# Kernel optimization log

Measured on AMD Instinct MI355X. Metric: run time of the kernel, lower is better.

Reference implementation:

```python
import jax, jax.numpy as jnp
import numpy as np

B, N = 4, 65536
NUM_GROUP, GROUP_SIZE = 512, 64
EMB = 60


def setup_inputs() -> dict:
    key = jax.random.key(0)
    ks = jax.random.split(key, 8)
    inp = {
        'xyz': jax.random.uniform(ks[0], (B, N, 3), jnp.float32),
        'color': jax.random.uniform(ks[1], (B, N, 3), jnp.float32),
        'W1': jax.random.normal(ks[2], (6, 64), jnp.float32) * 0.2,
        'b1': jnp.zeros((64,), jnp.float32),
        'W2': jax.random.normal(ks[3], (64, 128), jnp.float32) * 0.1,
        'b2': jnp.zeros((128,), jnp.float32),
        'W3': jax.random.normal(ks[4], (128, 256), jnp.float32) * 0.08,
        'b3': jnp.zeros((256,), jnp.float32),
        'W4': jax.random.normal(ks[5], (256, 512), jnp.float32) * 0.06,
        'b4': jnp.zeros((512,), jnp.float32),
        'Wp': jax.random.normal(ks[6], (512, EMB), jnp.float32) * 0.04,
        'bp': jnp.zeros((EMB,), jnp.float32),
    }
    return inp


def fps(xyz, n):
    """Farthest point sampling. xyz: (B,N,3) -> centers (B,n,3)."""
    b, npts, _ = xyz.shape
    start = jnp.zeros((b,), jnp.int32)
    d0 = jnp.full((b, npts), 1e10, xyz.dtype)

    def step(carry, _):
        dists, last = carry
        p = jnp.take_along_axis(xyz, last[:, None, None], axis=1)  # (B,1,3)
        d = jnp.sum((xyz - p) ** 2, axis=-1)                       # (B,N)
        dists = jnp.minimum(dists, d)
        nxt = jnp.argmax(dists, axis=-1).astype(jnp.int32)
        return (dists, nxt), nxt

    (_, _), rest = jax.lax.scan(step, (d0, start), None, length=n - 1)
    idx = jnp.concatenate([start[:, None], rest.T], axis=1)        # (B,n)
    return jax.vmap(lambda pts, i: pts[i])(xyz, idx)


def knn_idx(k, xyz, new_xyz):
    """Indices of k nearest points in xyz for each query in new_xyz.
    xyz: (B,N,3), new_xyz: (B,S,3) -> (B,S,k) int32. Matches
    square_distance + topk(largest=False)."""
    sq = (jnp.sum(new_xyz ** 2, -1)[..., None]
          + jnp.sum(xyz ** 2, -1)[:, None, :]
          - 2.0 * jnp.einsum('bsc,bnc->bsn', new_xyz, xyz))        # (B,S,N)
    _, idx = jax.lax.top_k(-sq, k)
    return idx


def reference(xyz, color, W1, b1, W2, b2, W3, b3, W4, b4, Wp, bp):
    # --- Group: FPS centers + KNN neighborhood gather + centering ---
    center = fps(xyz, NUM_GROUP)                                   # (B,G,3)
    idx = knn_idx(GROUP_SIZE, xyz, center)                         # (B,G,M)
    gather = jax.vmap(lambda pts, i: pts[i])                       # pts[(B,)N,3], i (G,M)
    neighborhood = gather(xyz, idx) - center[:, :, None, :]        # (B,G,M,3) centered
    neighborhood_color = gather(color, idx)                        # (B,G,M,3)
    feats = jnp.concatenate([neighborhood, neighborhood_color], -1)  # (B,G,M,6)

    # --- PointNet: per-point MLP -> max over group -> projection ---
    x = jax.nn.relu(feats @ W1 + b1)
    x = jax.nn.relu(x @ W2 + b2)
    x = jax.nn.relu(x @ W3 + b3)
    x = jax.nn.relu(x @ W4 + b4)                                   # (B,G,M,512)
    x = jnp.max(x, axis=2)                                         # (B,G,512)
    emb = x @ Wp + bp                                              # (B,G,60)
    return emb, center
```

## Files before the change

kernel.cpp:

```cpp
#include <hip/hip_runtime.h>
#include <stdint.h>

#define DI __device__ __forceinline__

typedef _Float16 f16x8 __attribute__((ext_vector_type(8)));
typedef float f32x4 __attribute__((ext_vector_type(4)));

constexpr int kB = 4;
constexpr int kN = 65536;
constexpr int kG = 512;
constexpr int kM = 64;
constexpr int kE = 60;
constexpr int GRD = 20;
constexpr int NCELL = GRD * GRD * GRD;
constexpr float CW = 1.0f / 20.0f;

constexpr int FPS_SUB = 8;
constexpr int FPS_PT_T = kN / FPS_SUB / 1024;

constexpr size_t OFF_WIN    = 0;
constexpr size_t OFF_CNT    = OFF_WIN + (size_t)kB * kG * 8;
constexpr size_t OFF_CCNT   = OFF_CNT + (size_t)kB * kG * 4;
constexpr size_t ZERO_BYTES = OFF_CCNT + (size_t)kB * NCELL * 4;
constexpr size_t OFF_CSTART = ZERO_BYTES;
constexpr size_t OFF_CUR    = OFF_CSTART + (size_t)kB * (NCELL + 1) * 4;
constexpr size_t OFF_SW1    = ((OFF_CUR + (size_t)kB * NCELL * 4) + 255) & ~(size_t)255;
constexpr size_t OFF_SW2    = OFF_SW1 + 2048 * 2;
constexpr size_t OFF_SW3    = OFF_SW2 + 8192 * 2;
constexpr size_t OFF_SW4    = OFF_SW3 + 32768 * 2;
constexpr size_t OFF_WPT    = OFF_SW4 + 131072 * 2;
constexpr size_t OFF_SORT   = ((OFF_WPT + 60 * 512 * 4) + 255) & ~(size_t)255;
constexpr size_t OFF_KIDX   = OFF_SORT + (size_t)kB * kN * 16;

DI int cellof(float x) {
  int c = (int)(x * (float)GRD);
  return min(GRD - 1, max(0, c));
}
DI unsigned orderable(float f) {
  unsigned u = __float_as_uint(f);
  return (u & 0x80000000u) ? ~u : (u | 0x80000000u);
}

__global__ void k_zero(uint32_t* p, int nwords) {
  int i = blockIdx.x * blockDim.x + threadIdx.x;
  int st = gridDim.x * blockDim.x;
  for (; i < nwords; i += st) p[i] = 0u;
}

DI void swz(const float* __restrict__ W, _Float16* __restrict__ sw,
            int total, int nks, int Kreal, int N, int i0, int st) {
  for (int i = i0; i < total; i += st) {
    int j = i & 7, lane = (i >> 3) & 63, rest = i >> 9;
    int ks = rest % nks, nt = rest / nks;
    int k = ks * 32 + ((lane >> 4) << 3) + j;
    int n = nt * 16 + (lane & 15);
    sw[i] = (_Float16)((k < Kreal) ? W[k * N + n] : 0.f);
  }
}

__global__ void k_prep(const float* __restrict__ W1, const float* __restrict__ W2,
                       const float* __restrict__ W3, const float* __restrict__ W4,
                       const float* __restrict__ Wp,
                       _Float16* __restrict__ sw1, _Float16* __restrict__ sw2,
                       _Float16* __restrict__ sw3, _Float16* __restrict__ sw4,
                       float* __restrict__ wpt) {
  int i0 = blockIdx.x * blockDim.x + threadIdx.x;
  int st = gridDim.x * blockDim.x;
  swz(W1, sw1, 2048, 1, 6, 64, i0, st);
  swz(W2, sw2, 8192, 2, 64, 128, i0, st);
  swz(W3, sw3, 32768, 4, 128, 256, i0, st);
  swz(W4, sw4, 131072, 8, 256, 512, i0, st);
  for (int i = i0; i < 60 * 512; i += st) { int n = i >> 9, k = i & 511; wpt[i] = Wp[k * 60 + n]; }
}

__global__ __launch_bounds__(1024) void k_fps(const float* __restrict__ xyz,
                                              float* __restrict__ outC,
                                              unsigned long long* __restrict__ win,
                                              unsigned int* __restrict__ cnt) {
  const int b = blockIdx.x >> 3, sub = blockIdx.x & 7;
  const int tid = threadIdx.x;
  const float* X = xyz + (size_t)b * kN * 3;
  float px[FPS_PT_T], py[FPS_PT_T], pz[FPS_PT_T], dd[FPS_PT_T];
#pragma unroll
  for (int j = 0; j < FPS_PT_T; ++j) {
    int p = sub * (kN / FPS_SUB) + j * 1024 + tid;
    px[j] = X[3 * p]; py[j] = X[3 * p + 1]; pz[j] = X[3 * p + 2];
    dd[j] = 1e10f;
  }
  float lx = X[0], ly = X[1], lz = X[2];
  if (sub == 0 && tid == 0) {
    outC[(size_t)b * kG * 3 + 0] = lx;
    outC[(size_t)b * kG * 3 + 1] = ly;
    outC[(size_t)b * kG * 3 + 2] = lz;
  }
  __shared__ unsigned long long wres[16];
  __shared__ float sp[3];
  unsigned long long* winB = win + (size_t)b * kG;
  unsigned int* cntB = cnt + (size_t)b * kG;

  for (int it = 1; it < kG; ++it) {
    unsigned long long best = 0ull;
#pragma unroll
    for (int j = 0; j < FPS_PT_T; ++j) {
      float dx = __fsub_rn(px[j], lx);
      float dy = __fsub_rn(py[j], ly);
      float dz = __fsub_rn(pz[j], lz);
      float d = __fadd_rn(__fadd_rn(__fmul_rn(dx, dx), __fmul_rn(dy, dy)), __fmul_rn(dz, dz));
      float nd = fminf(dd[j], d);
      dd[j] = nd;
      int p = sub * (kN / FPS_SUB) + j * 1024 + tid;
      unsigned long long pk =
          ((unsigned long long)__float_as_uint(nd) << 32) | (unsigned)(0xFFFFFFFFu - (unsigned)p);
      best = (pk > best) ? pk : best;
    }
#pragma unroll
    for (int off = 32; off; off >>= 1) {
      unsigned long long o = __shfl_down(best, (unsigned)off);
      best = (o > best) ? o : best;
    }
    if ((tid & 63) == 0) wres[tid >> 6] = best;
    __syncthreads();
    if (tid == 0) {
      unsigned long long bb = wres[0];
#pragma unroll
      for (int i = 1; i < 16; ++i) bb = (wres[i] > bb) ? wres[i] : bb;
      atomicMax(winB + it, bb | (1ull << 63));
      __threadfence();
      atomicAdd(cntB + it, 1u);
      long bail = 0;
      while (__hip_atomic_load(cntB + it, __ATOMIC_ACQUIRE, __HIP_MEMORY_SCOPE_AGENT) < (unsigned)FPS_SUB) {
        __builtin_amdgcn_s_sleep(1);
        if (++bail > 100000000L) break;
      }
      unsigned long long w = __hip_atomic_load(winB + it, __ATOMIC_ACQUIRE, __HIP_MEMORY_SCOPE_AGENT);
      int wi = (int)(0xFFFFFFFFu - (unsigned)(w & 0xFFFFFFFFu));
      float wx = X[3 * wi], wy = X[3 * wi + 1], wz = X[3 * wi + 2];
      sp[0] = wx; sp[1] = wy; sp[2] = wz;
      if (sub == 0) {
        outC[((size_t)b * kG + it) * 3 + 0] = wx;
        outC[((size_t)b * kG + it) * 3 + 1] = wy;
        outC[((size_t)b * kG + it) * 3 + 2] = wz;
      }
    }
    __syncthreads();
    lx = sp[0]; ly = sp[1]; lz = sp[2];
  }
}

__global__ void k_cellcount(const float* __restrict__ xyz, uint32_t* __restrict__ ccnt) {
  int i = blockIdx.x * blockDim.x + threadIdx.x;
  int st = gridDim.x * blockDim.x;
  for (; i < kB * kN; i += st) {
    int b = i >> 16, p = i & (kN - 1);
    const float* q = xyz + ((size_t)b * kN + p) * 3;
    int cid = (cellof(q[2]) * GRD + cellof(q[1])) * GRD + cellof(q[0]);
    atomicAdd(&ccnt[b * NCELL + cid], 1u);
  }
}

__global__ void k_scan(const uint32_t* __restrict__ ccnt, uint32_t* __restrict__ cstart,
                       uint32_t* __restrict__ cur) {
  int b = blockIdx.x, tid = threadIdx.x;
  const uint32_t* cc = ccnt + (size_t)b * NCELL;
  uint32_t* cs = cstart + (size_t)b * (NCELL + 1);
  uint32_t* cu = cur + (size_t)b * NCELL;
  __shared__ uint32_t part[256];
  const int chunk = 32;
  int c0 = tid * chunk;
  uint32_t s = 0;
  for (int i = 0; i < chunk; ++i) { int c = c0 + i; if (c < NCELL) s += cc[c]; }
  part[tid] = s;
  __syncthreads();
  for (int off = 1; off < 256; off <<= 1) {
    uint32_t add = (tid >= off) ? part[tid - off] : 0u;
    __syncthreads();
    part[tid] += add;
    __syncthreads();
  }
  uint32_t run = part[tid] - s;
  for (int i = 0; i < chunk; ++i) {
    int c = c0 + i;
    if (c < NCELL) { cs[c] = run; cu[c] = run; run += cc[c]; }
  }
  if (tid == 255) cs[NCELL] = run;
}

__global__ void k_scatter(const float* __restrict__ xyz, uint32_t* __restrict__ cur,
                          float4* __restrict__ sorted) {
  int i = blockIdx.x * blockDim.x + threadIdx.x;
  int st = gridDim.x * blockDim.x;
  for (; i < kB * kN; i += st) {
    int b = i >> 16, p = i & (kN - 1);
    const float* q = xyz + ((size_t)b * kN + p) * 3;
    float x = q[0], y = q[1], z = q[2];
    int cid = (cellof(z) * GRD + cellof(y)) * GRD + cellof(x);
    uint32_t pos = atomicAdd(&cur[b * NCELL + cid], 1u);
    sorted[(size_t)b * kN + pos] = make_float4(x, y, z, __uint_as_float((unsigned)p));
  }
}

constexpr int CAP = 8192;

DI void bitonic(unsigned long long* a, int n, int tid) {
  for (int k = 2; k <= n; k <<= 1)
    for (int j = k >> 1; j > 0; j >>= 1) {
      __syncthreads();
      for (int i = tid; i < n; i += 256) {
        int ix = i ^ j;
        if (ix > i) {
          unsigned long long x = a[i], y = a[ix];
          bool up = ((i & k) == 0);
          if ((x > y) == up) { a[i] = y; a[ix] = x; }
        }
      }
    }
  __syncthreads();
}

__global__ __launch_bounds__(256) void k_knn(const float4* __restrict__ sorted,
                                             const uint32_t* __restrict__ cstart,
                                             const float* __restrict__ outC,
                                             uint32_t* __restrict__ kidx) {
  const int bi = blockIdx.x;
  const int b = (bi & 7) >> 1;
  const int g = ((bi >> 3) << 1) | (bi & 1);
  const int tid = threadIdx.x;
  __shared__ unsigned long long cand[CAP];
  __shared__ int nC;
  const float cx = outC[((size_t)b * kG + g) * 3 + 0];
  const float cy = outC[((size_t)b * kG + g) * 3 + 1];
  const float cz = outC[((size_t)b * kG + g) * 3 + 2];
  const float nc = __fadd_rn(__fadd_rn(__fmul_rn(cx, cx), __fmul_rn(cy, cy)), __fmul_rn(cz, cz));
  const float4* SP = sorted + (size_t)b * kN;
  const uint32_t* CS = cstart + (size_t)b * (NCELL + 1);
  const int ccx = cellof(cx), ccy = cellof(cy), ccz = cellof(cz);
  if (tid == 0) nC = 0;
  __syncthreads();
  int plox = 1, phix = 0, ploy = 1, phiy = 0, ploz = 1, phiz = 0;
  for (int r = 1; r <= GRD; ++r) {
    int lox = max(0, ccx - r), hix = min(GRD - 1, ccx + r);
    int loy = max(0, ccy - r), hiy = min(GRD - 1, ccy + r);
    int loz = max(0, ccz - r), hiz = min(GRD - 1, ccz + r);
    for (int z = loz; z <= hiz; ++z)
      for (int y = loy; y <= hiy; ++y) {
        bool rowPrev = (r > 1) && (z >= ploz && z <= phiz && y >= ploy && y <= phiy);
        for (int s = 0; s < 2; ++s) {
          int xa, xb;
          if (!rowPrev) { if (s) break; xa = lox; xb = hix; }
          else if (s == 0) { xa = lox; xb = plox - 1; }
          else { xa = phix + 1; xb = hix; }
          if (xa > xb) continue;
          int c0 = (z * GRD + y) * GRD + xa;
          int i0 = CS[c0];
          int i1 = CS[(z * GRD + y) * GRD + xb + 1];
          for (int i = i0 + tid; i < i1; i += 256) {
            float4 pt = SP[i];
            float npn = __fadd_rn(__fadd_rn(__fmul_rn(pt.x, pt.x), __fmul_rn(pt.y, pt.y)),
                                  __fmul_rn(pt.z, pt.z));
            float dot = __fadd_rn(__fadd_rn(__fmul_rn(cx, pt.x), __fmul_rn(cy, pt.y)),
                                  __fmul_rn(cz, pt.z));
            float sq = __fsub_rn(__fadd_rn(nc, npn), __fmul_rn(2.0f, dot));
            unsigned key = orderable(sq);
            int pos = atomicAdd(&nC, 1);
            if (pos < CAP)
              cand[pos] = ((unsigned long long)key << 32) | (unsigned)__float_as_uint(pt.w);
          }
        }
      }
    __syncthreads();
    int n = min(nC, CAP);
    float rc = 1e30f;
    if (lox > 0) rc = fminf(rc, cx - (float)lox * CW);
    if (hix < GRD - 1) rc = fminf(rc, (float)(hix + 1) * CW - cx);
    if (loy > 0) rc = fminf(rc, cy - (float)loy * CW);
    if (hiy < GRD - 1) rc = fminf(rc, (float)(hiy + 1) * CW - cy);
    if (loz > 0) rc = fminf(rc, cz - (float)loz * CW);
    if (hiz < GRD - 1) rc = fminf(rc, (float)(hiz + 1) * CW - cz);
    float r2 = (rc >= 1e29f) ? 3.0e38f : rc * rc * (1.0f - 1e-5f);
    unsigned keyR = orderable(r2);
    bool done = false;
    if (n >= kM) {
      int np2 = 1;
      while (np2 < n) np2 <<= 1;
      for (int i = n + tid; i < np2; i += 256) cand[i] = ~0ull;
      bitonic(cand, np2, tid);
      unsigned k63 = (unsigned)(cand[kM - 1] >> 32);
      done = (k63 <= keyR);
      if (tid == 0) nC = n;
    }
    __syncthreads();
    if (done) break;
    plox = lox; phix = hix; ploy = loy; phiy = hiy; ploz = loz; phiz = hiz;
  }
  if (tid < kM)
    kidx[((size_t)b * kG + g) * kM + tid] = (uint32_t)(cand[tid] & 0xFFFFFFFFu);
}


template <int Kdim, int Ndim, int SIN, int SOUT>
DI void mfma_layer(const _Float16* __restrict__ Xin, _Float16* __restrict__ Xout,
                   const _Float16* __restrict__ Wsw, const float* __restrict__ bias,
                   int wave, int lane) {
  constexpr int NKS = Kdim / 32;
  constexpr int NTW = Ndim / 64;
  constexpr int CH = (NTW < 4) ? NTW : 4;
  const int quad = lane >> 4, l16 = lane & 15;
  for (int c0 = 0; c0 < NTW; c0 += CH) {
    f32x4 acc[CH][4];
#pragma unroll
    for (int nt = 0; nt < CH; ++nt) {
      float bv = bias[wave * (Ndim / 4) + (c0 + nt) * 16 + l16];
#pragma unroll
      for (int m = 0; m < 4; ++m) acc[nt][m] = {bv, bv, bv, bv};
    }
#pragma unroll
    for (int ks = 0; ks < NKS; ++ks) {
      f16x8 af[4];
#pragma unroll
      for (int m = 0; m < 4; ++m)
        af[m] = *(const f16x8*)(Xin + (m * 16 + l16) * SIN + ks * 32 + quad * 8);
#pragma unroll
      for (int nt = 0; nt < CH; ++nt) {
        int ntg = wave * NTW + c0 + nt;
        f16x8 bf = *(const f16x8*)(Wsw + ((size_t)(ntg * NKS + ks) * 64 + lane) * 8);
#pragma unroll
        for (int m = 0; m < 4; ++m)
          acc[nt][m] = __builtin_amdgcn_mfma_f32_16x16x32_f16(af[m], bf, acc[nt][m], 0, 0, 0);
      }
    }
#pragma unroll
    for (int nt = 0; nt < CH; ++nt) {
      int col = wave * (Ndim / 4) + (c0 + nt) * 16 + l16;
#pragma unroll
      for (int m = 0; m < 4; ++m)
#pragma unroll
        for (int r = 0; r < 4; ++r) {
          int row = m * 16 + quad * 4 + r;
          Xout[row * SOUT + col] = (_Float16)fmaxf(acc[nt][m][r], 0.f);
        }
    }
  }
}

DI void mfma_layer4(const _Float16* __restrict__ Xin, const _Float16* __restrict__ Wsw,
                    const float* __restrict__ bias, float* __restrict__ maxv,
                    int wave, int lane) {
  constexpr int SIN = 264, NKS = 8, NTW = 8, CH = 4;
  const int quad = lane >> 4, l16 = lane & 15;
  for (int c0 = 0; c0 < NTW; c0 += CH) {
    f32x4 acc[CH][4];
#pragma unroll
    for (int nt = 0; nt < CH; ++nt) {
      float bv = bias[wave * 128 + (c0 + nt) * 16 + l16];
#pragma unroll
      for (int m = 0; m < 4; ++m) acc[nt][m] = {bv, bv, bv, bv};
    }
#pragma unroll
    for (int ks = 0; ks < NKS; ++ks) {
      f16x8 af[4];
#pragma unroll
      for (int m = 0; m < 4; ++m)
        af[m] = *(const f16x8*)(Xin + (m * 16 + l16) * SIN + ks * 32 + quad * 8);
#pragma unroll
      for (int nt = 0; nt < CH; ++nt) {
        int ntg = wave * NTW + c0 + nt;
        f16x8 bf = *(const f16x8*)(Wsw + ((size_t)(ntg * NKS + ks) * 64 + lane) * 8);
#pragma unroll
        for (int m = 0; m < 4; ++m)
          acc[nt][m] = __builtin_amdgcn_mfma_f32_16x16x32_f16(af[m], bf, acc[nt][m], 0, 0, 0);
      }
    }
#pragma unroll
    for (int nt = 0; nt < CH; ++nt) {
      float mx = 0.f;
#pragma unroll
      for (int m = 0; m < 4; ++m)
#pragma unroll
        for (int r = 0; r < 4; ++r) mx = fmaxf(mx, acc[nt][m][r]);
      mx = fmaxf(mx, __shfl_xor(mx, 16, 64));
      mx = fmaxf(mx, __shfl_xor(mx, 32, 64));
      if (quad == 0) maxv[wave * 128 + (c0 + nt) * 16 + l16] = mx;
    }
  }
}

__global__ __launch_bounds__(256) void k_mlp(
    const float* __restrict__ xyz, const float* __restrict__ color,
    const float* __restrict__ outC, const uint32_t* __restrict__ kidx,
    const _Float16* __restrict__ sw1, const _Float16* __restrict__ sw2,
    const _Float16* __restrict__ sw3, const _Float16* __restrict__ sw4,
    const float* __restrict__ wpt,
    const float* __restrict__ b1, const float* __restrict__ b2,
    const float* __restrict__ b3, const float* __restrict__ b4,
    const float* __restrict__ bp, float* __restrict__ outE) {
  const int bi = blockIdx.x;
  const int b = (bi & 7) >> 1;
  const int g = ((bi >> 3) << 1) | (bi & 1);
  const int tid = threadIdx.x;
  const int wave = tid >> 6, lane = tid & 63;
  __shared__ __align__(16) char smem[17408 + 33792];
  _Float16* bufA = (_Float16*)smem;
  _Float16* bufB = (_Float16*)(smem + 17408);
  float* maxv = (float*)smem;
  float* psum = (float*)(smem + 2048);

  if (tid < kM) {
    uint32_t p = kidx[((size_t)b * kG + g) * kM + tid];
    const float* cen = outC + ((size_t)b * kG + g) * 3;
    const float* xp = xyz + ((size_t)b * kN + p) * 3;
    const float* cp = color + ((size_t)b * kN + p) * 3;
    f16x8 v = {};
    v[0] = (_Float16)__fsub_rn(xp[0], cen[0]);
    v[1] = (_Float16)__fsub_rn(xp[1], cen[1]);
    v[2] = (_Float16)__fsub_rn(xp[2], cen[2]);
    v[3] = (_Float16)cp[0];
    v[4] = (_Float16)cp[1];
    v[5] = (_Float16)cp[2];
    f16x8 z = {};
    *(f16x8*)(bufA + tid * 40 + 0) = v;
    *(f16x8*)(bufA + tid * 40 + 8) = z;
    *(f16x8*)(bufA + tid * 40 + 16) = z;
    *(f16x8*)(bufA + tid * 40 + 24) = z;
  }
  __syncthreads();
  mfma_layer<32, 64, 40, 72>(bufA, bufB, sw1, b1, wave, lane);
  __syncthreads();
  mfma_layer<64, 128, 72, 136>(bufB, bufA, sw2, b2, wave, lane);
  __syncthreads();
  mfma_layer<128, 256, 136, 264>(bufA, bufB, sw3, b3, wave, lane);
  __syncthreads();
  mfma_layer4(bufB, sw4, b4, maxv, wave, lane);
  __syncthreads();
  if (tid < 240) {
    int j = tid >> 2, q = tid & 3;
    const float* w = wpt + (size_t)j * 512 + q * 128;
    float s = 0.f;
#pragma unroll 4
    for (int k = 0; k < 128; ++k) s = fmaf(maxv[q * 128 + k], w[k], s);
    psum[tid] = s;
  }
  __syncthreads();
  if (tid < kE) {
    float e = __fadd_rn(__fadd_rn(psum[tid * 4 + 0], psum[tid * 4 + 1]),
                        __fadd_rn(psum[tid * 4 + 2], psum[tid * 4 + 3])) + bp[tid];
    outE[((size_t)b * kG + g) * kE + tid] = e;
  }
}

extern "C" void kernel_launch(void* const* d_in, const int* in_sizes, int n_in,
                              void* d_out, int out_size, void* d_ws, size_t ws_size,
                              hipStream_t stream) {
  (void)in_sizes; (void)n_in; (void)out_size; (void)ws_size;
  const float* xyz = (const float*)d_in[0];
  const float* color = (const float*)d_in[1];
  const float* W1 = (const float*)d_in[2];
  const float* b1 = (const float*)d_in[3];
  const float* W2 = (const float*)d_in[4];
  const float* b2 = (const float*)d_in[5];
  const float* W3 = (const float*)d_in[6];
  const float* b3 = (const float*)d_in[7];
  const float* W4 = (const float*)d_in[8];
  const float* b4 = (const float*)d_in[9];
  const float* Wp = (const float*)d_in[10];
  const float* bp = (const float*)d_in[11];

  char* ws = (char*)d_ws;
  auto win = (unsigned long long*)(ws + OFF_WIN);
  auto cnt = (unsigned int*)(ws + OFF_CNT);
  auto ccnt = (uint32_t*)(ws + OFF_CCNT);
  auto cstart = (uint32_t*)(ws + OFF_CSTART);
  auto cur = (uint32_t*)(ws + OFF_CUR);
  auto sw1 = (_Float16*)(ws + OFF_SW1);
  auto sw2 = (_Float16*)(ws + OFF_SW2);
  auto sw3 = (_Float16*)(ws + OFF_SW3);
  auto sw4 = (_Float16*)(ws + OFF_SW4);
  auto wpt = (float*)(ws + OFF_WPT);
  auto sorted = (float4*)(ws + OFF_SORT);
  auto kidx = (uint32_t*)(ws + OFF_KIDX);

  float* outE = (float*)d_out;
  float* outC = outE + (size_t)kB * kG * kE;

  k_zero<<<64, 256, 0, stream>>>((uint32_t*)ws, (int)(ZERO_BYTES / 4));
  k_prep<<<256, 256, 0, stream>>>(W1, W2, W3, W4, Wp, sw1, sw2, sw3, sw4, wpt);
  k_fps<<<kB * FPS_SUB, 1024, 0, stream>>>(xyz, outC, win, cnt);
  k_cellcount<<<512, 256, 0, stream>>>(xyz, ccnt);
  k_scan<<<kB, 256, 0, stream>>>(ccnt, cstart, cur);
  k_scatter<<<512, 256, 0, stream>>>(xyz, cur, sorted);
  k_knn<<<kB * kG, 256, 0, stream>>>(sorted, cstart, outC, kidx);
  k_mlp<<<kB * kG, 256, 0, stream>>>(xyz, color, outC, kidx, sw1, sw2, sw3, sw4, wpt,
                                     b1, b2, b3, b4, bp, outE);
}
```

Before: 1.998 ms.

## Replace FPS atomic counter barrier with per-block slot exchange and doubled block split

```diff
diff --git a/kernel.cpp b/kernel.cpp
--- a/kernel.cpp
+++ b/kernel.cpp
@@ -15,14 +15,13 @@
 constexpr int NCELL = GRD * GRD * GRD;
 constexpr float CW = 1.0f / 20.0f;
 
-constexpr int FPS_SUB = 8;
+constexpr int FPS_SUB = 16;
 constexpr int FPS_PT_T = kN / FPS_SUB / 1024;
 
-constexpr size_t OFF_WIN    = 0;
-constexpr size_t OFF_CNT    = OFF_WIN + (size_t)kB * kG * 8;
-constexpr size_t OFF_CCNT   = OFF_CNT + (size_t)kB * kG * 4;
+constexpr size_t OFF_FKEY   = 0;
+constexpr size_t OFF_CCNT   = OFF_FKEY + (size_t)kB * kG * FPS_SUB * 4 * 8;
 constexpr size_t ZERO_BYTES = OFF_CCNT + (size_t)kB * NCELL * 4;
-constexpr size_t OFF_CSTART = ZERO_BYTES;
+constexpr size_t OFF_CSTART = (ZERO_BYTES + 255) & ~(size_t)255;
 constexpr size_t OFF_CUR    = OFF_CSTART + (size_t)kB * (NCELL + 1) * 4;
 constexpr size_t OFF_SW1    = ((OFF_CUR + (size_t)kB * NCELL * 4) + 255) & ~(size_t)255;
 constexpr size_t OFF_SW2    = OFF_SW1 + 2048 * 2;
@@ -75,10 +74,10 @@
 
 __global__ __launch_bounds__(1024) void k_fps(const float* __restrict__ xyz,
                                               float* __restrict__ outC,
-                                              unsigned long long* __restrict__ win,
-                                              unsigned int* __restrict__ cnt) {
-  const int b = blockIdx.x >> 3, sub = blockIdx.x & 7;
+                                              unsigned long long* __restrict__ fkey) {
+  const int b = blockIdx.x / FPS_SUB, sub = blockIdx.x % FPS_SUB;
   const int tid = threadIdx.x;
+  const int wave = tid >> 6, lane = tid & 63;
   const float* X = xyz + (size_t)b * kN * 3;
   float px[FPS_PT_T], py[FPS_PT_T], pz[FPS_PT_T], dd[FPS_PT_T];
 #pragma unroll
@@ -93,13 +92,14 @@
     outC[(size_t)b * kG * 3 + 1] = ly;
     outC[(size_t)b * kG * 3 + 2] = lz;
   }
-  __shared__ unsigned long long wres[16];
-  __shared__ float sp[3];
-  unsigned long long* winB = win + (size_t)b * kG;
-  unsigned int* cntB = cnt + (size_t)b * kG;
+  __shared__ unsigned long long wkey[16];
+  __shared__ float wx[16], wy[16], wz[16];
+  __shared__ float4 sp;
+  unsigned long long* keyB = fkey + (size_t)b * kG * FPS_SUB * 4;
 
   for (int it = 1; it < kG; ++it) {
     unsigned long long best = 0ull;
+    float bx = 0.f, by = 0.f, bz = 0.f;
 #pragma unroll
     for (int j = 0; j < FPS_PT_T; ++j) {
       float dx = __fsub_rn(px[j], lx);
@@ -111,39 +111,75 @@
       int p = sub * (kN / FPS_SUB) + j * 1024 + tid;
       unsigned long long pk =
           ((unsigned long long)__float_as_uint(nd) << 32) | (unsigned)(0xFFFFFFFFu - (unsigned)p);
-      best = (pk > best) ? pk : best;
+      if (pk > best) { best = pk; bx = px[j]; by = py[j]; bz = pz[j]; }
     }
 #pragma unroll
     for (int off = 32; off; off >>= 1) {
-      unsigned long long o = __shfl_down(best, (unsigned)off);
-      best = (o > best) ? o : best;
-    }
-    if ((tid & 63) == 0) wres[tid >> 6] = best;
+      unsigned long long ok = __shfl_down(best, (unsigned)off);
+      float ox = __shfl_down(bx, (unsigned)off);
+      float oy = __shfl_down(by, (unsigned)off);
+      float oz = __shfl_down(bz, (unsigned)off);
+      if (ok > best) { best = ok; bx = ox; by = oy; bz = oz; }
+    }
+    if (lane == 0) { wkey[wave] = best; wx[wave] = bx; wy[wave] = by; wz[wave] = bz; }
     __syncthreads();
-    if (tid == 0) {
-      unsigned long long bb = wres[0];
-#pragma unroll
-      for (int i = 1; i < 16; ++i) bb = (wres[i] > bb) ? wres[i] : bb;
-      atomicMax(winB + it, bb | (1ull << 63));
-      __threadfence();
-      atomicAdd(cntB + it, 1u);
+    if (wave == 0) {
+      int i16 = lane & 15;
+      unsigned long long kk = wkey[i16];
+      float kx = wx[i16], ky = wy[i16], kz = wz[i16];
+#pragma unroll
+      for (int off = 8; off; off >>= 1) {
+        unsigned long long ok = __shfl_down(kk, (unsigned)off);
+        float ox = __shfl_down(kx, (unsigned)off);
+        float oy = __shfl_down(ky, (unsigned)off);
+        float oz = __shfl_down(kz, (unsigned)off);
+        if (ok > kk) { kk = ok; kx = ox; ky = oy; kz = oz; }
+      }
+      unsigned long long* slots = keyB + (size_t)it * (FPS_SUB * 4);
+      if (lane == 0) {
+        unsigned long long tag = (unsigned)it;
+        unsigned long long* my = slots + sub * 4;
+        __hip_atomic_store(my + 1, ((unsigned long long)__float_as_uint(kx) << 32) | tag,
+                           __ATOMIC_RELAXED, __HIP_MEMORY_SCOPE_AGENT);
+        __hip_atomic_store(my + 2, ((unsigned long long)__float_as_uint(ky) << 32) | tag,
+                           __ATOMIC_RELAXED, __HIP_MEMORY_SCOPE_AGENT);
+        __hip_atomic_store(my + 3, ((unsigned long long)__float_as_uint(kz) << 32) | tag,
+                           __ATOMIC_RELAXED, __HIP_MEMORY_SCOPE_AGENT);
+        __hip_atomic_store(my + 0, kk, __ATOMIC_RELAXED, __HIP_MEMORY_SCOPE_AGENT);
+      }
+      unsigned long long v;
+      bool ok;
       long bail = 0;
-      while (__hip_atomic_load(cntB + it, __ATOMIC_ACQUIRE, __HIP_MEMORY_SCOPE_AGENT) < (unsigned)FPS_SUB) {
-        __builtin_amdgcn_s_sleep(1);
-        if (++bail > 100000000L) break;
-      }
-      unsigned long long w = __hip_atomic_load(winB + it, __ATOMIC_ACQUIRE, __HIP_MEMORY_SCOPE_AGENT);
-      int wi = (int)(0xFFFFFFFFu - (unsigned)(w & 0xFFFFFFFFu));
-      float wx = X[3 * wi], wy = X[3 * wi + 1], wz = X[3 * wi + 2];
-      sp[0] = wx; sp[1] = wy; sp[2] = wz;
-      if (sub == 0) {
-        outC[((size_t)b * kG + it) * 3 + 0] = wx;
-        outC[((size_t)b * kG + it) * 3 + 1] = wy;
-        outC[((size_t)b * kG + it) * 3 + 2] = wz;
+      do {
+        v = __hip_atomic_load(slots + lane, __ATOMIC_RELAXED, __HIP_MEMORY_SCOPE_AGENT);
+        ok = (lane & 3) ? ((unsigned)v == (unsigned)it) : (v != 0ull);
+      } while (!__all(ok) && ++bail < 100000000L);
+      unsigned long long key = (lane & 3) ? 0ull : v;
+      int slot = lane >> 2;
+#pragma unroll
+      for (int off = 32; off; off >>= 1) {
+        unsigned long long ok2 = __shfl_down(key, (unsigned)off);
+        int os = __shfl_down(slot, (unsigned)off);
+        if (ok2 > key) { key = ok2; slot = os; }
+      }
+      slot = __shfl(slot, 0);
+      unsigned long long vx = __shfl(v, slot * 4 + 1);
+      unsigned long long vy = __shfl(v, slot * 4 + 2);
+      unsigned long long vz = __shfl(v, slot * 4 + 3);
+      if (lane == 0) {
+        float wxc = __uint_as_float((unsigned)(vx >> 32));
+        float wyc = __uint_as_float((unsigned)(vy >> 32));
+        float wzc = __uint_as_float((unsigned)(vz >> 32));
+        sp = make_float4(wxc, wyc, wzc, 0.f);
+        if (sub == 0) {
+          outC[((size_t)b * kG + it) * 3 + 0] = wxc;
+          outC[((size_t)b * kG + it) * 3 + 1] = wyc;
+          outC[((size_t)b * kG + it) * 3 + 2] = wzc;
+        }
       }
     }
     __syncthreads();
-    lx = sp[0]; ly = sp[1]; lz = sp[2];
+    lx = sp.x; ly = sp.y; lz = sp.z;
   }
 }
 
@@ -465,8 +501,7 @@
   const float* bp = (const float*)d_in[11];
 
   char* ws = (char*)d_ws;
-  auto win = (unsigned long long*)(ws + OFF_WIN);
-  auto cnt = (unsigned int*)(ws + OFF_CNT);
+  auto fkey = (unsigned long long*)(ws + OFF_FKEY);
   auto ccnt = (uint32_t*)(ws + OFF_CCNT);
   auto cstart = (uint32_t*)(ws + OFF_CSTART);
   auto cur = (uint32_t*)(ws + OFF_CUR);
@@ -481,9 +516,9 @@
   float* outE = (float*)d_out;
   float* outC = outE + (size_t)kB * kG * kE;
 
-  k_zero<<<64, 256, 0, stream>>>((uint32_t*)ws, (int)(ZERO_BYTES / 4));
+  k_zero<<<128, 256, 0, stream>>>((uint32_t*)ws, (int)(ZERO_BYTES / 4));
   k_prep<<<256, 256, 0, stream>>>(W1, W2, W3, W4, Wp, sw1, sw2, sw3, sw4, wpt);
-  k_fps<<<kB * FPS_SUB, 1024, 0, stream>>>(xyz, outC, win, cnt);
+  k_fps<<<kB * FPS_SUB, 1024, 0, stream>>>(xyz, outC, fkey);
   k_cellcount<<<512, 256, 0, stream>>>(xyz, ccnt);
   k_scan<<<kB, 256, 0, stream>>>(ccnt, cstart, cur);
   k_scatter<<<512, 256, 0, stream>>>(xyz, cur, sorted);
```

Result: slower. 2.257 ms (+13.0%).
